# Kernel tuning notes

Hardware: AMD Instinct MI355X
Metric: run time of the kernel (lower is better)

Reference implementation:

```python
import jax, jax.numpy as jnp
import numpy as np

T, N, D, E, O = 2, 4096, 1024, 8, 1024

def setup_inputs() -> dict:
    key = jax.random.key(0)
    k1, k2, k3 = jax.random.split(key, 3)
    x = jax.random.normal(k1, (T, N, D), dtype=jnp.float32)
    Wg = jax.random.normal(k2, (T, D, E), dtype=jnp.float32) * (1.0 / np.sqrt(D))
    We = jax.random.normal(k3, (E, D, O), dtype=jnp.float32) * (1.0 / np.sqrt(D))
    return {"x": x, "Wg": Wg, "We": We, "k": 2}


def reference(x, Wg, We, k):
    # Per-task gating logits: [T, N, E]
    logits = jnp.einsum('tnd,tde->tne', x, Wg)
    # Top-k mask per token (scatter 1.0 at top-k indices)
    _, topk_idx = jax.lax.top_k(logits, k)                      # [T, N, k]
    mask = jax.nn.one_hot(topk_idx, E, dtype=logits.dtype).sum(-2)  # [T, N, E]
    masked = mask * logits
    gates = masked / (masked.sum(-1, keepdims=True) + 1e-9)     # [T, N, E]
    # Dense expert outputs (each expert is Linear(D, O)): [T, N, E, O]
    eout = jnp.einsum('tnd,edo->tneo', x, We)
    # Weighted combine over selected experts
    out = jnp.einsum('tne,tneo->tno', gates, eout)              # [T, N, O]
    return out
```

## Files before the change

kernel.cpp:

```cpp
#include <hip/hip_runtime.h>
#include <hip/hip_bf16.h>
#include <stdint.h>

#define T_ 2
#define N_ 4096
#define D_ 1024
#define E_ 8
#define O_ 1024

#define BM 128
#define BN 128
#define BK 32

typedef __attribute__((ext_vector_type(8))) short short8;
typedef __attribute__((ext_vector_type(4))) float f32x4;

#define AS1 __attribute__((address_space(1)))
#define AS3 __attribute__((address_space(3)))

__device__ inline void gld16(const unsigned short* g, unsigned short* l) {
    __builtin_amdgcn_global_load_lds((const AS1 unsigned int*)g,
                                     (AS3 unsigned int*)l, 16, 0, 0);
}

__device__ inline unsigned short f2bf(float f) {
    union { float f; unsigned u; } v; v.f = f;
    unsigned r = v.u + 0x7fff + ((v.u >> 16) & 1);
    return (unsigned short)(r >> 16);
}

__global__ __launch_bounds__(256) void gate_kernel(
    const float* __restrict__ x, const float* __restrict__ Wg,
    unsigned short* __restrict__ xb,
    int* __restrict__ route, float2* __restrict__ gpair)
{
    __shared__ __align__(16) float WgT[E_][D_];

    int tid = threadIdx.x;
    int wave = tid >> 6, lane = tid & 63;
    int token0 = blockIdx.x * 32;
    int t = token0 >> 12;
    const float* wgb = Wg + (size_t)t * D_ * E_;

#pragma unroll
    for (int r = 0; r < 8; ++r) {
        int f = r * 1024 + tid * 4;
        float4 v = *(const float4*)(wgb + f);
        WgT[f & 7][f >> 3]             = v.x;
        WgT[(f + 1) & 7][(f + 1) >> 3] = v.y;
        WgT[(f + 2) & 7][(f + 2) >> 3] = v.z;
        WgT[(f + 3) & 7][(f + 3) >> 3] = v.w;
    }
    __syncthreads();

    for (int tl = 0; tl < 8; ++tl) {
        int token = token0 + wave * 8 + tl;
        const float* xrow = x + (size_t)token * D_;

        float4 xv[4];
#pragma unroll
        for (int c = 0; c < 4; ++c)
            xv[c] = *(const float4*)(xrow + c * 256 + lane * 4);

        float acc[E_] = {0.f, 0.f, 0.f, 0.f, 0.f, 0.f, 0.f, 0.f};
#pragma unroll
        for (int c = 0; c < 4; ++c) {
            int d0 = c * 256 + lane * 4;
            unsigned lo = f2bf(xv[c].x) | ((unsigned)f2bf(xv[c].y) << 16);
            unsigned hi = f2bf(xv[c].z) | ((unsigned)f2bf(xv[c].w) << 16);
            *(uint2*)(&xb[(size_t)token * D_ + d0]) = make_uint2(lo, hi);
#pragma unroll
            for (int e = 0; e < E_; ++e) {
                float4 w = *(const float4*)(&WgT[e][d0]);
                acc[e] += xv[c].x * w.x + xv[c].y * w.y + xv[c].z * w.z + xv[c].w * w.w;
            }
        }
#pragma unroll
        for (int off = 1; off < 64; off <<= 1) {
#pragma unroll
            for (int e = 0; e < E_; ++e) acc[e] += __shfl_xor(acc[e], off, 64);
        }

        if (lane == 0) {
            float best = acc[0]; int bi = 0;
#pragma unroll
            for (int e = 1; e < E_; ++e) if (acc[e] > best) { best = acc[e]; bi = e; }
            float sec = -INFINITY; int si = 0;
#pragma unroll
            for (int e = 0; e < E_; ++e) if (e != bi && acc[e] > sec) { sec = acc[e]; si = e; }
            float s = best + sec + 1e-9f;
            route[token] = bi | (si << 8);
            gpair[token] = make_float2(best / s, sec / s);
        }
    }
}

__global__ __launch_bounds__(256) void build_lists(
    const int* __restrict__ route, const float2* __restrict__ gpair,
    int* __restrict__ toklist, float* __restrict__ gatelist,
    int* __restrict__ counts)
{
    int g = blockIdx.x;
    int t = g >> 3, e = g & 7;
    int tid = threadIdx.x;
    int wave = tid >> 6, lane = tid & 63;

    __shared__ int waveSum[4];
    __shared__ int base;
    if (tid == 0) base = 0;

    for (int c = 0; c < N_; c += 256) {
        int n = c + tid;
        int r = route[t * N_ + n];
        int e0 = r & 255, e1 = (r >> 8) & 255;
        bool sel = (e0 == e) || (e1 == e);
        unsigned long long b = __ballot(sel);
        int pre  = __popcll(b & ((1ull << lane) - 1ull));
        if (lane == 0) waveSum[wave] = __popcll(b);
        __syncthreads();
        int woff = 0;
#pragma unroll
        for (int w = 0; w < 4; ++w) woff += (w < wave) ? waveSum[w] : 0;
        int total = waveSum[0] + waveSum[1] + waveSum[2] + waveSum[3];
        if (sel) {
            int p = base + woff + pre;
            int slot = (e0 == e) ? 0 : 1;
            toklist[g * N_ + p] = n | (slot << 16);
            float2 gp = gpair[t * N_ + n];
            gatelist[g * N_ + p] = (e0 == e) ? gp.x : gp.y;
        }
        __syncthreads();
        if (tid == 0) base += total;
    }
    __syncthreads();
    if (tid == 0) counts[g] = base;
}

__global__ __launch_bounds__(256) void pack_kernel(
    const float* __restrict__ We, unsigned short* __restrict__ Wbp)
{
    __shared__ __align__(16) unsigned short P[64 * 136];

    int b = blockIdx.x;
    int e  = b >> 7;
    int oy = (b & 127) >> 3;
    int dz = b & 7;
    int o0 = oy * 64, d0 = dz * 128;
    int tid = threadIdx.x;

#pragma unroll
    for (int r = 0; r < 32; ++r) {
        int lin = r * 256 + tid;
        int dd = lin >> 6, oo = lin & 63;
        P[oo * 136 + dd] = f2bf(We[((size_t)(e * D_ + d0 + dd)) * O_ + o0 + oo]);
    }
    __syncthreads();

#pragma unroll
    for (int w = 0; w < 4; ++w) {
        int ci = w * 256 + tid;
        int oo = ci >> 4, dc = ci & 15;
        uint4 v = *(const uint4*)&P[oo * 136 + dc * 8];
        int o = o0 + oo;
        int ot = o >> 7, nn = o & 127;
        unsigned short* dst =
            Wbp + ((size_t)((e * 8 + ot) * 128 + nn)) * D_ + d0 + dc * 8;
        *(uint4*)dst = v;
    }
}

__global__ __launch_bounds__(256) void moe_gemm(
    const unsigned short* __restrict__ xb,
    const unsigned short* __restrict__ Wbp,
    const int* __restrict__ toklist, const float* __restrict__ gatelist,
    const int* __restrict__ counts, float* __restrict__ out)
{
    int lin = blockIdx.x + (blockIdx.y << 5) + (blockIdx.z << 8);
    int xcd = lin & 7, slot_ = lin >> 3;
    int mt = slot_ & 31;
    int pr = xcd * 16 + (slot_ >> 5);
    int ot = pr & 7;
    int g  = pr >> 3;
    int t  = g >> 3;

    int cnt = counts[g];
    int m0 = mt * BM;
    if (m0 >= cnt) return;

    __shared__ __align__(16) unsigned short As[BM * 32];
    __shared__ __align__(16) unsigned short Bs[BN * 32];
    __shared__ int   tokS[BM];
    __shared__ float gateS[BM];

    int tid = threadIdx.x;
    if (tid < BM) {
        int r = m0 + tid;
        tokS[tid]  = (r < cnt) ? toklist[g * N_ + r]  : -1;
        gateS[tid] = (r < cnt) ? gatelist[g * N_ + r] : 0.f;
    }
    __syncthreads();

    int wave = tid >> 6, lane = tid & 63;
    int lr = lane >> 2;
    int lc = (lane & 3) * 8;
    int c0 = wave * 2, c1 = c0 + 1;
    int ar0 = c0 * 16 + lr, ar1 = c1 * 16 + lr;
    int tok0 = max(tokS[ar0], 0) & 0xFFFF;
    int tok1 = max(tokS[ar1], 0) & 0xFFFF;
    const unsigned short* ag0 = xb + ((size_t)(t * N_ + tok0)) * D_ + lc;
    const unsigned short* ag1 = xb + ((size_t)(t * N_ + tok1)) * D_ + lc;
    const unsigned short* wb  = Wbp + ((size_t)((g & 7) * 8 + ot) * 128) * D_;
    const unsigned short* bg0 = wb + (size_t)ar0 * D_ + lc;
    const unsigned short* bg1 = wb + (size_t)ar1 * D_ + lc;
    unsigned short* la0 = &As[c0 * 16 * 32];
    unsigned short* la1 = &As[c1 * 16 * 32];
    unsigned short* lb0 = &Bs[c0 * 16 * 32];
    unsigned short* lb1 = &Bs[c1 * 16 * 32];

    int wm = (wave & 1) * 64, wn = (wave >> 1) * 64;
    int fr = lane & 15, q = lane >> 4;

    f32x4 acc[4][4];
#pragma unroll
    for (int mi = 0; mi < 4; ++mi)
#pragma unroll
        for (int ni = 0; ni < 4; ++ni) acc[mi][ni] = (f32x4){0.f, 0.f, 0.f, 0.f};

    for (int k0 = 0; k0 < D_; k0 += BK) {
        gld16(ag0 + k0, la0);
        gld16(ag1 + k0, la1);
        gld16(bg0 + k0, lb0);
        gld16(bg1 + k0, lb1);
        __syncthreads();

        short8 af[4], bf[4];
#pragma unroll
        for (int mi = 0; mi < 4; ++mi)
            af[mi] = *(const short8*)(&As[(wm + mi * 16 + fr) * 32 + q * 8]);
#pragma unroll
        for (int ni = 0; ni < 4; ++ni)
            bf[ni] = *(const short8*)(&Bs[(wn + ni * 16 + fr) * 32 + q * 8]);
#pragma unroll
        for (int mi = 0; mi < 4; ++mi)
#pragma unroll
            for (int ni = 0; ni < 4; ++ni)
                acc[mi][ni] = __builtin_amdgcn_mfma_f32_16x16x32_bf16(
                    af[mi], bf[ni], acc[mi][ni], 0, 0, 0);
        __syncthreads();
    }

    float* outb = out + (size_t)t * N_ * O_;
    int ncol = ot * 128 + wn + fr;
#pragma unroll
    for (int mi = 0; mi < 4; ++mi) {
#pragma unroll
        for (int r = 0; r < 4; ++r) {
            int ml = wm + mi * 16 + q * 4 + r;
            int ent = tokS[ml];
            if (ent >= 0) {
                int tok  = ent & 0xFFFF;
                int slot = ent >> 16;
                float gate = gateS[ml];
#pragma unroll
                for (int ni = 0; ni < 4; ++ni) {
                    unsigned short* p =
                        (unsigned short*)(outb + (size_t)tok * O_ + ncol + ni * 16);
                    p[slot] = f2bf(gate * acc[mi][ni][r]);
                }
            }
        }
    }
}

__global__ __launch_bounds__(256) void combine_kernel(float* __restrict__ out)
{
    size_t i = ((size_t)blockIdx.x * 256 + threadIdx.x) * 4;
    unsigned* po = (unsigned*)out;
    uint4 v = *(uint4*)(po + i);
    float4 r;
    union { unsigned u; float f; } a, b;
#define CMB(comp, src) a.u = (src) << 16; b.u = (src) & 0xFFFF0000u; comp = a.f + b.f
    CMB(r.x, v.x); CMB(r.y, v.y); CMB(r.z, v.z); CMB(r.w, v.w);
#undef CMB
    *(float4*)(out + i) = r;
}

extern "C" void kernel_launch(void* const* d_in, const int* in_sizes, int n_in,
                              void* d_out, int out_size, void* d_ws, size_t ws_size,
                              hipStream_t stream)
{
    const float* x  = (const float*)d_in[0];
    const float* Wg = (const float*)d_in[1];
    const float* We = (const float*)d_in[2];
    float* out = (float*)d_out;

    char* ws = (char*)d_ws;
    unsigned short* xb   = (unsigned short*)(ws);
    unsigned short* Wbp  = (unsigned short*)(ws + 16777216);
    int*   toklist       = (int*)  (ws + 33554432);
    float* gatelist      = (float*)(ws + 33816576);
    int*   counts        = (int*)  (ws + 34078720);
    int*   route         = (int*)  (ws + 34078976);
    float2* gpair        = (float2*)(ws + 34111744);

    gate_kernel<<<(T_ * N_) / 32, 256, 0, stream>>>(x, Wg, xb, route, gpair);
    build_lists<<<T_ * E_, 256, 0, stream>>>(route, gpair, toklist, gatelist, counts);
    pack_kernel<<<E_ * (O_ / 64) * (D_ / 128), 256, 0, stream>>>(We, Wbp);
    moe_gemm<<<dim3(N_ / BM, O_ / BN, T_ * E_), 256, 0, stream>>>(
        xb, Wbp, toklist, gatelist, counts, out);
    combine_kernel<<<((size_t)T_ * N_ * O_) / (256 * 4), 256, 0, stream>>>(out);
}
```

Before: 203.2 us.

## Use persistent work-queue MoE GEMM with BK=64 swizzled LDS and finer gate grid

Replaces the sparse 3D grid with early-exit blocks by a fixed persistent grid that walks a compacted list of non-empty tiles (prefix sums of per-group tile counts) and pulls further work through an atomic counter reset in build_lists. The K tile is doubled to 64, and LDS rows use an XOR swizzle to cut bank conflicts while halving the number of barriers per tile. The gate kernel is split into four times as many blocks, each handling fewer tokens, to raise parallelism. The costs are an atomic and barrier per work item, more LDS per block under launch bounds of 4 blocks, and a redundant Wg load into LDS by every gate block.

```diff
diff --git a/kernel.cpp b/kernel.cpp
--- a/kernel.cpp
+++ b/kernel.cpp
@@ -10,7 +10,8 @@
 
 #define BM 128
 #define BN 128
-#define BK 32
+#define BK 64
+#define GEMM_GRID 1024
 
 typedef __attribute__((ext_vector_type(8))) short short8;
 typedef __attribute__((ext_vector_type(4))) float f32x4;
@@ -38,7 +39,7 @@
 
     int tid = threadIdx.x;
     int wave = tid >> 6, lane = tid & 63;
-    int token0 = blockIdx.x * 32;
+    int token0 = blockIdx.x * 8;
     int t = token0 >> 12;
     const float* wgb = Wg + (size_t)t * D_ * E_;
 
@@ -53,8 +54,9 @@
     }
     __syncthreads();
 
-    for (int tl = 0; tl < 8; ++tl) {
-        int token = token0 + wave * 8 + tl;
+#pragma unroll
+    for (int tl = 0; tl < 2; ++tl) {
+        int token = token0 + wave * 2 + tl;
         const float* xrow = x + (size_t)token * D_;
 
         float4 xv[4];
@@ -98,12 +100,13 @@
 __global__ __launch_bounds__(256) void build_lists(
     const int* __restrict__ route, const float2* __restrict__ gpair,
     int* __restrict__ toklist, float* __restrict__ gatelist,
-    int* __restrict__ counts)
+    int* __restrict__ counts, int* __restrict__ workctr)
 {
     int g = blockIdx.x;
     int t = g >> 3, e = g & 7;
     int tid = threadIdx.x;
     int wave = tid >> 6, lane = tid & 63;
+    if (g == 0 && tid == 0) *workctr = GEMM_GRID;
 
     __shared__ int waveSum[4];
     __shared__ int base;
@@ -169,106 +172,129 @@
     }
 }
 
-__global__ __launch_bounds__(256) void moe_gemm(
+__global__ __launch_bounds__(256, 4) void moe_gemm(
     const unsigned short* __restrict__ xb,
     const unsigned short* __restrict__ Wbp,
     const int* __restrict__ toklist, const float* __restrict__ gatelist,
-    const int* __restrict__ counts, float* __restrict__ out)
-{
-    int lin = blockIdx.x + (blockIdx.y << 5) + (blockIdx.z << 8);
-    int xcd = lin & 7, slot_ = lin >> 3;
-    int mt = slot_ & 31;
-    int pr = xcd * 16 + (slot_ >> 5);
-    int ot = pr & 7;
-    int g  = pr >> 3;
-    int t  = g >> 3;
-
-    int cnt = counts[g];
-    int m0 = mt * BM;
-    if (m0 >= cnt) return;
-
-    __shared__ __align__(16) unsigned short As[BM * 32];
-    __shared__ __align__(16) unsigned short Bs[BN * 32];
+    const int* __restrict__ counts, int* __restrict__ workctr,
+    float* __restrict__ out)
+{
+    __shared__ __align__(16) unsigned short As[BM * BK];
+    __shared__ __align__(16) unsigned short Bs[BN * BK];
     __shared__ int   tokS[BM];
     __shared__ float gateS[BM];
+    __shared__ int   cntS[16], mtp[17];
+    __shared__ int   curIdx;
 
     int tid = threadIdx.x;
-    if (tid < BM) {
-        int r = m0 + tid;
-        tokS[tid]  = (r < cnt) ? toklist[g * N_ + r]  : -1;
-        gateS[tid] = (r < cnt) ? gatelist[g * N_ + r] : 0.f;
-    }
-    __syncthreads();
-
     int wave = tid >> 6, lane = tid & 63;
-    int lr = lane >> 2;
-    int lc = (lane & 3) * 8;
-    int c0 = wave * 2, c1 = c0 + 1;
-    int ar0 = c0 * 16 + lr, ar1 = c1 * 16 + lr;
-    int tok0 = max(tokS[ar0], 0) & 0xFFFF;
-    int tok1 = max(tokS[ar1], 0) & 0xFFFF;
-    const unsigned short* ag0 = xb + ((size_t)(t * N_ + tok0)) * D_ + lc;
-    const unsigned short* ag1 = xb + ((size_t)(t * N_ + tok1)) * D_ + lc;
-    const unsigned short* wb  = Wbp + ((size_t)((g & 7) * 8 + ot) * 128) * D_;
-    const unsigned short* bg0 = wb + (size_t)ar0 * D_ + lc;
-    const unsigned short* bg1 = wb + (size_t)ar1 * D_ + lc;
-    unsigned short* la0 = &As[c0 * 16 * 32];
-    unsigned short* la1 = &As[c1 * 16 * 32];
-    unsigned short* lb0 = &Bs[c0 * 16 * 32];
-    unsigned short* lb1 = &Bs[c1 * 16 * 32];
-
+
+    if (tid < 16) cntS[tid] = counts[tid];
+    __syncthreads();
+    if (tid == 0) {
+        int s = 0; mtp[0] = 0;
+#pragma unroll
+        for (int g = 0; g < 16; ++g) { s += (cntS[g] + BM - 1) >> 7; mtp[g + 1] = s; }
+    }
+    __syncthreads();
+    int totalItems = mtp[16] * 8;
+
+    int lr = lane >> 3;
+    int sg = (lane & 7) ^ lr;
+    int fr = lane & 15, q = lane >> 4;
     int wm = (wave & 1) * 64, wn = (wave >> 1) * 64;
-    int fr = lane & 15, q = lane >> 4;
-
-    f32x4 acc[4][4];
-#pragma unroll
-    for (int mi = 0; mi < 4; ++mi)
-#pragma unroll
-        for (int ni = 0; ni < 4; ++ni) acc[mi][ni] = (f32x4){0.f, 0.f, 0.f, 0.f};
-
-    for (int k0 = 0; k0 < D_; k0 += BK) {
-        gld16(ag0 + k0, la0);
-        gld16(ag1 + k0, la1);
-        gld16(bg0 + k0, lb0);
-        gld16(bg1 + k0, lb1);
+
+    int idx = blockIdx.x;
+    while (idx < totalItems) {
+        int tile = idx >> 3, ot = idx & 7;
+        int g = 0;
+        while (mtp[g + 1] <= tile) ++g;
+        int t = g >> 3;
+        int cnt = cntS[g];
+        int m0 = (tile - mtp[g]) * BM;
+
+        if (tid < BM) {
+            int r = m0 + tid;
+            tokS[tid]  = (r < cnt) ? toklist[g * N_ + r]  : -1;
+            gateS[tid] = (r < cnt) ? gatelist[g * N_ + r] : 0.f;
+        }
         __syncthreads();
 
-        short8 af[4], bf[4];
+        const unsigned short* ag[4];
+        const unsigned short* bg[4];
+        const unsigned short* wb = Wbp + ((size_t)((g & 7) * 8 + ot) * 128) * D_;
+#pragma unroll
+        for (int i = 0; i < 4; ++i) {
+            int row = (wave * 4 + i) * 8 + lr;
+            int tok = max(tokS[row], 0) & 0xFFFF;
+            ag[i] = xb + ((size_t)(t * N_ + tok)) * D_ + sg * 8;
+            bg[i] = wb + (size_t)row * D_ + sg * 8;
+        }
+        unsigned short* la = &As[wave * 4 * 512];
+        unsigned short* lb = &Bs[wave * 4 * 512];
+
+        f32x4 acc[4][4];
 #pragma unroll
         for (int mi = 0; mi < 4; ++mi)
-            af[mi] = *(const short8*)(&As[(wm + mi * 16 + fr) * 32 + q * 8]);
-#pragma unroll
-        for (int ni = 0; ni < 4; ++ni)
-            bf[ni] = *(const short8*)(&Bs[(wn + ni * 16 + fr) * 32 + q * 8]);
-#pragma unroll
-        for (int mi = 0; mi < 4; ++mi)
-#pragma unroll
-            for (int ni = 0; ni < 4; ++ni)
-                acc[mi][ni] = __builtin_amdgcn_mfma_f32_16x16x32_bf16(
-                    af[mi], bf[ni], acc[mi][ni], 0, 0, 0);
-        __syncthreads();
-    }
-
-    float* outb = out + (size_t)t * N_ * O_;
-    int ncol = ot * 128 + wn + fr;
-#pragma unroll
-    for (int mi = 0; mi < 4; ++mi) {
-#pragma unroll
-        for (int r = 0; r < 4; ++r) {
-            int ml = wm + mi * 16 + q * 4 + r;
-            int ent = tokS[ml];
-            if (ent >= 0) {
-                int tok  = ent & 0xFFFF;
-                int slot = ent >> 16;
-                float gate = gateS[ml];
+#pragma unroll
+            for (int ni = 0; ni < 4; ++ni) acc[mi][ni] = (f32x4){0.f, 0.f, 0.f, 0.f};
+
+        for (int k0 = 0; k0 < D_; k0 += BK) {
+#pragma unroll
+            for (int i = 0; i < 4; ++i) {
+                gld16(ag[i] + k0, la + i * 512);
+                gld16(bg[i] + k0, lb + i * 512);
+            }
+            __syncthreads();
+
+#pragma unroll
+            for (int kk = 0; kk < 2; ++kk) {
+                short8 af[4], bf[4];
+#pragma unroll
+                for (int mi = 0; mi < 4; ++mi) {
+                    int r = wm + mi * 16 + fr;
+                    af[mi] = *(const short8*)(&As[r * BK + (((kk * 4 + q) ^ (fr & 7)) * 8)]);
+                }
 #pragma unroll
                 for (int ni = 0; ni < 4; ++ni) {
-                    unsigned short* p =
-                        (unsigned short*)(outb + (size_t)tok * O_ + ncol + ni * 16);
-                    p[slot] = f2bf(gate * acc[mi][ni][r]);
+                    int r = wn + ni * 16 + fr;
+                    bf[ni] = *(const short8*)(&Bs[r * BK + (((kk * 4 + q) ^ (fr & 7)) * 8)]);
+                }
+#pragma unroll
+                for (int mi = 0; mi < 4; ++mi)
+#pragma unroll
+                    for (int ni = 0; ni < 4; ++ni)
+                        acc[mi][ni] = __builtin_amdgcn_mfma_f32_16x16x32_bf16(
+                            af[mi], bf[ni], acc[mi][ni], 0, 0, 0);
+            }
+            __syncthreads();
+        }
+
+        float* outb = out + (size_t)t * N_ * O_;
+        int ncol = ot * 128 + wn + fr;
+#pragma unroll
+        for (int mi = 0; mi < 4; ++mi) {
+#pragma unroll
+            for (int r = 0; r < 4; ++r) {
+                int ml = wm + mi * 16 + q * 4 + r;
+                int ent = tokS[ml];
+                if (ent >= 0) {
+                    int tok  = ent & 0xFFFF;
+                    int slot = ent >> 16;
+                    float gate = gateS[ml];
+#pragma unroll
+                    for (int ni = 0; ni < 4; ++ni) {
+                        unsigned short* p =
+                            (unsigned short*)(outb + (size_t)tok * O_ + ncol + ni * 16);
+                        p[slot] = f2bf(gate * acc[mi][ni][r]);
+                    }
                 }
             }
         }
+
+        if (tid == 0) curIdx = atomicAdd(workctr, 1);
+        __syncthreads();
+        idx = curIdx;
     }
 }
 
@@ -300,13 +326,15 @@
     int*   toklist       = (int*)  (ws + 33554432);
     float* gatelist      = (float*)(ws + 33816576);
     int*   counts        = (int*)  (ws + 34078720);
-    int*   route         = (int*)  (ws + 34078976);
-    float2* gpair        = (float2*)(ws + 34111744);
-
-    gate_kernel<<<(T_ * N_) / 32, 256, 0, stream>>>(x, Wg, xb, route, gpair);
-    build_lists<<<T_ * E_, 256, 0, stream>>>(route, gpair, toklist, gatelist, counts);
+    int*   workctr       = (int*)  (ws + 34078976);
+    int*   route         = (int*)  (ws + 34079232);
+    float2* gpair        = (float2*)(ws + 34112000);
+
+    gate_kernel<<<(T_ * N_) / 8, 256, 0, stream>>>(x, Wg, xb, route, gpair);
+    build_lists<<<T_ * E_, 256, 0, stream>>>(route, gpair, toklist, gatelist,
+                                             counts, workctr);
     pack_kernel<<<E_ * (O_ / 64) * (D_ / 128), 256, 0, stream>>>(We, Wbp);
-    moe_gemm<<<dim3(N_ / BM, O_ / BN, T_ * E_), 256, 0, stream>>>(
-        xb, Wbp, toklist, gatelist, counts, out);
+    moe_gemm<<<GEMM_GRID, 256, 0, stream>>>(xb, Wbp, toklist, gatelist,
+                                            counts, workctr, out);
     combine_kernel<<<((size_t)T_ * N_ * O_) / (256 * 4), 256, 0, stream>>>(out);
 }
```

After: 251.6 us. 1.24x slower.

## Swizzle LDS tiles, reorder GEMM block mapping, and spread gating over more blocks

Applied to the files above, without the earlier changes.

The GEMM now XOR-swizzles the 16-byte chunks of each 32-wide bf16 row in LDS, for both the global-to-LDS writes and the fragment reads, to avoid bank conflicts. It also switches to a 1D grid whose mapping puts the M tile in the high bits, so every block for a given (group, output tile) pair stays on the same XCD, which may improve L2 reuse of the weight tiles. Separately, the gating kernel now handles 8 tokens per block instead of 32, giving four times as many blocks, with each block still reloading the full Wg slice into LDS.

```diff
diff --git a/kernel.cpp b/kernel.cpp
--- a/kernel.cpp
+++ b/kernel.cpp
@@ -38,7 +38,7 @@
 
     int tid = threadIdx.x;
     int wave = tid >> 6, lane = tid & 63;
-    int token0 = blockIdx.x * 32;
+    int token0 = blockIdx.x * 8;
     int t = token0 >> 12;
     const float* wgb = Wg + (size_t)t * D_ * E_;
 
@@ -53,8 +53,9 @@
     }
     __syncthreads();
 
-    for (int tl = 0; tl < 8; ++tl) {
-        int token = token0 + wave * 8 + tl;
+#pragma unroll
+    for (int tl = 0; tl < 2; ++tl) {
+        int token = token0 + wave * 2 + tl;
         const float* xrow = x + (size_t)token * D_;
 
         float4 xv[4];
@@ -175,20 +176,21 @@
     const int* __restrict__ toklist, const float* __restrict__ gatelist,
     const int* __restrict__ counts, float* __restrict__ out)
 {
-    int lin = blockIdx.x + (blockIdx.y << 5) + (blockIdx.z << 8);
-    int xcd = lin & 7, slot_ = lin >> 3;
-    int mt = slot_ & 31;
-    int pr = xcd * 16 + (slot_ >> 5);
-    int ot = pr & 7;
-    int g  = pr >> 3;
-    int t  = g >> 3;
+    int lin = blockIdx.x;
+    int mt  = lin >> 7;
+    int u   = lin & 127;
+    int xcd = u & 7;
+    int v   = u >> 3;
+    int g   = 2 * xcd + (v >> 3);
+    int ot  = v & 7;
+    int t   = g >> 3;
 
     int cnt = counts[g];
     int m0 = mt * BM;
     if (m0 >= cnt) return;
 
-    __shared__ __align__(16) unsigned short As[BM * 32];
-    __shared__ __align__(16) unsigned short Bs[BN * 32];
+    __shared__ __align__(16) unsigned short As[BM * BK];
+    __shared__ __align__(16) unsigned short Bs[BN * BK];
     __shared__ int   tokS[BM];
     __shared__ float gateS[BM];
 
@@ -202,23 +204,24 @@
 
     int wave = tid >> 6, lane = tid & 63;
     int lr = lane >> 2;
-    int lc = (lane & 3) * 8;
+    int sg = (lane & 3) ^ (lr & 3);
     int c0 = wave * 2, c1 = c0 + 1;
     int ar0 = c0 * 16 + lr, ar1 = c1 * 16 + lr;
     int tok0 = max(tokS[ar0], 0) & 0xFFFF;
     int tok1 = max(tokS[ar1], 0) & 0xFFFF;
-    const unsigned short* ag0 = xb + ((size_t)(t * N_ + tok0)) * D_ + lc;
-    const unsigned short* ag1 = xb + ((size_t)(t * N_ + tok1)) * D_ + lc;
+    const unsigned short* ag0 = xb + ((size_t)(t * N_ + tok0)) * D_ + sg * 8;
+    const unsigned short* ag1 = xb + ((size_t)(t * N_ + tok1)) * D_ + sg * 8;
     const unsigned short* wb  = Wbp + ((size_t)((g & 7) * 8 + ot) * 128) * D_;
-    const unsigned short* bg0 = wb + (size_t)ar0 * D_ + lc;
-    const unsigned short* bg1 = wb + (size_t)ar1 * D_ + lc;
-    unsigned short* la0 = &As[c0 * 16 * 32];
-    unsigned short* la1 = &As[c1 * 16 * 32];
-    unsigned short* lb0 = &Bs[c0 * 16 * 32];
-    unsigned short* lb1 = &Bs[c1 * 16 * 32];
-
+    const unsigned short* bg0 = wb + (size_t)ar0 * D_ + sg * 8;
+    const unsigned short* bg1 = wb + (size_t)ar1 * D_ + sg * 8;
+    unsigned short* la0 = &As[c0 * 512];
+    unsigned short* la1 = &As[c1 * 512];
+    unsigned short* lb0 = &Bs[c0 * 512];
+    unsigned short* lb1 = &Bs[c1 * 512];
+
+    int fr = lane & 15, q = lane >> 4;
     int wm = (wave & 1) * 64, wn = (wave >> 1) * 64;
-    int fr = lane & 15, q = lane >> 4;
+    int fp = (q ^ (fr & 3)) * 8;
 
     f32x4 acc[4][4];
 #pragma unroll
@@ -236,10 +239,10 @@
         short8 af[4], bf[4];
 #pragma unroll
         for (int mi = 0; mi < 4; ++mi)
-            af[mi] = *(const short8*)(&As[(wm + mi * 16 + fr) * 32 + q * 8]);
+            af[mi] = *(const short8*)(&As[(wm + mi * 16 + fr) * BK + fp]);
 #pragma unroll
         for (int ni = 0; ni < 4; ++ni)
-            bf[ni] = *(const short8*)(&Bs[(wn + ni * 16 + fr) * 32 + q * 8]);
+            bf[ni] = *(const short8*)(&Bs[(wn + ni * 16 + fr) * BK + fp]);
 #pragma unroll
         for (int mi = 0; mi < 4; ++mi)
 #pragma unroll
@@ -303,10 +306,10 @@
     int*   route         = (int*)  (ws + 34078976);
     float2* gpair        = (float2*)(ws + 34111744);
 
-    gate_kernel<<<(T_ * N_) / 32, 256, 0, stream>>>(x, Wg, xb, route, gpair);
+    gate_kernel<<<(T_ * N_) / 8, 256, 0, stream>>>(x, Wg, xb, route, gpair);
     build_lists<<<T_ * E_, 256, 0, stream>>>(route, gpair, toklist, gatelist, counts);
     pack_kernel<<<E_ * (O_ / 64) * (D_ / 128), 256, 0, stream>>>(We, Wbp);
-    moe_gemm<<<dim3(N_ / BM, O_ / BN, T_ * E_), 256, 0, stream>>>(
+    moe_gemm<<<(N_ / BM) * 8 * (T_ * E_), 256, 0, stream>>>(
         xb, Wbp, toklist, gatelist, counts, out);
     combine_kernel<<<((size_t)T_ * N_ * O_) / (256 * 4), 256, 0, stream>>>(out);
 }
```

Measured after the change: 194.7 us. 1.04x faster.
